# Kernel tuning notes

Measured on AMD Instinct MI355X. Metric: run time of the kernel, lower is better.

Reference implementation:

```python
import jax, jax.numpy as jnp
import numpy as np

N = 16384       # num nodes
E = 65536       # num edges (before self loops)
IN_DIM = 1536
HID = 1024
HEADS = 8
HD = HID // HEADS  # 128
NEG_SLOPE = 0.2
EPS = 1e-5


def _xavier(key, shape):
    fan_in, fan_out = shape[0], shape[-1]
    s = jnp.sqrt(6.0 / (fan_in + fan_out)).astype(jnp.float32)
    return jax.random.uniform(key, shape, jnp.float32, -s, s)


def setup_inputs() -> dict:
    key = jax.random.key(0)
    ks = jax.random.split(key, 32)
    inp = {
        "x": jax.random.normal(ks[0], (N, IN_DIM), jnp.float32),
        "edge_index": jax.random.randint(ks[1], (2, E), 0, N, dtype=jnp.int32),
        # input projection + norm1
        "W_in": _xavier(ks[2], (IN_DIM, HID)), "b_in": jnp.zeros((HID,), jnp.float32),
        "ln1_g": jnp.ones((HID,), jnp.float32), "ln1_b": jnp.zeros((HID,), jnp.float32),
        # GATv2 layer 1
        "g1_Wl": _xavier(ks[3], (HID, HID)), "g1_bl": jnp.zeros((HID,), jnp.float32),
        "g1_Wr": _xavier(ks[4], (HID, HID)), "g1_br": jnp.zeros((HID,), jnp.float32),
        "g1_att": _xavier(ks[5], (HEADS, HD)), "g1_bo": jnp.zeros((HID,), jnp.float32),
        "ln2_g": jnp.ones((HID,), jnp.float32), "ln2_b": jnp.zeros((HID,), jnp.float32),
        # GATv2 layer 2
        "g2_Wl": _xavier(ks[6], (HID, HID)), "g2_bl": jnp.zeros((HID,), jnp.float32),
        "g2_Wr": _xavier(ks[7], (HID, HID)), "g2_br": jnp.zeros((HID,), jnp.float32),
        "g2_att": _xavier(ks[8], (HEADS, HD)), "g2_bo": jnp.zeros((HID,), jnp.float32),
        "ln3_g": jnp.ones((HID,), jnp.float32), "ln3_b": jnp.zeros((HID,), jnp.float32),
        # scorer MLP 1024 -> 512 -> 128 -> 1
        "Ws1": _xavier(ks[9], (HID, 512)), "bs1": jnp.zeros((512,), jnp.float32),
        "Ws2": _xavier(ks[10], (512, 128)), "bs2": jnp.zeros((128,), jnp.float32),
        "Ws3": _xavier(ks[11], (128, 1)), "bs3": jnp.zeros((1,), jnp.float32),
    }
    return inp


def layer_norm(x, g, b):
    mu = jnp.mean(x, axis=-1, keepdims=True)
    var = jnp.var(x, axis=-1, keepdims=True)
    return (x - mu) * jax.lax.rsqrt(var + EPS) * g + b


def gatv2(h, src, dst, Wl, bl, Wr, br, att, bo):
    # GATv2Conv: x_j = lin_l(h)[src], x_i = lin_r(h)[dst]
    xl = (h @ Wl + bl).reshape(N, HEADS, HD)
    xr = (h @ Wr + br).reshape(N, HEADS, HD)
    e = jax.nn.leaky_relu(xl[src] + xr[dst], NEG_SLOPE)      # [E', H, C]
    logit = jnp.einsum('ehc,hc->eh', e, att)                  # [E', H]
    m = jax.ops.segment_max(logit, dst, num_segments=N)       # segment softmax over dst
    a = jnp.exp(logit - m[dst])
    denom = jax.ops.segment_sum(a, dst, num_segments=N)
    alpha = a / denom[dst]
    out = jax.ops.segment_sum(alpha[:, :, None] * xl[src], dst, num_segments=N)
    return out.reshape(N, HID) + bo


def reference(x, edge_index, W_in, b_in, ln1_g, ln1_b,
              g1_Wl, g1_bl, g1_Wr, g1_br, g1_att, g1_bo, ln2_g, ln2_b,
              g2_Wl, g2_bl, g2_Wr, g2_br, g2_att, g2_bo, ln3_g, ln3_b,
              Ws1, bs1, Ws2, bs2, Ws3, bs3):
    # PyG GATv2Conv adds self-loops by default
    loop = jnp.arange(N, dtype=edge_index.dtype)
    src = jnp.concatenate([edge_index[0], loop])
    dst = jnp.concatenate([edge_index[1], loop])

    h = jax.nn.gelu(layer_norm(x @ W_in + b_in, ln1_g, ln1_b), approximate=False)
    h1 = gatv2(h, src, dst, g1_Wl, g1_bl, g1_Wr, g1_br, g1_att, g1_bo)
    h = h + jax.nn.gelu(layer_norm(h1, ln2_g, ln2_b), approximate=False)
    h2 = gatv2(h, src, dst, g2_Wl, g2_bl, g2_Wr, g2_br, g2_att, g2_bo)
    h = h + jax.nn.gelu(layer_norm(h2, ln3_g, ln3_b), approximate=False)

    s = jax.nn.silu(h @ Ws1 + bs1)
    s = jax.nn.silu(s @ Ws2 + bs2)
    scores = (s @ Ws3 + bs3).squeeze(-1)   # [N]
    return scores, h
```

## Files before the change

kernel.cpp:

```cpp
#include <hip/hip_runtime.h>
#include <hip/hip_bf16.h>
#include <math.h>

#define N_NODES 16384
#define E_EDGES 65536
#define ET (E_EDGES + N_NODES)
#define IN_DIM 1536
#define HID 1024
#define XSTR 2048

typedef __attribute__((ext_vector_type(8))) short bf16x8;
typedef __attribute__((ext_vector_type(4))) float f32x4;

__device__ __forceinline__ unsigned short f2b(float f) {
  unsigned int u = __float_as_uint(f);
  u = (u + 0x7FFFu + ((u >> 16) & 1u)) >> 16;
  return (unsigned short)u;
}

__device__ __forceinline__ float b2f(unsigned short u) {
  return __uint_as_float((unsigned int)u << 16);
}

__device__ __forceinline__ void gload_lds16(const void* g, void* l) {
  __builtin_amdgcn_global_load_lds((const __attribute__((address_space(1))) void*)g,
                                   (__attribute__((address_space(3))) void*)l, 16, 0, 0);
}

__device__ __forceinline__ float gelu_exact(float y) {
  return 0.5f * y * (1.0f + erff(y * 0.70710678118654752f));
}

__global__ void conv_bf16_kernel(const float* __restrict__ in, unsigned short* __restrict__ out, int n4) {
  int i = blockIdx.x * 256 + threadIdx.x;
  if (i < n4) {
    float4 v = ((const float4*)in)[i];
    ushort4 o;
    o.x = f2b(v.x); o.y = f2b(v.y); o.z = f2b(v.z); o.w = f2b(v.w);
    ((ushort4*)out)[i] = o;
  }
}

__global__ void transpose_conv_kernel(const float* __restrict__ in, unsigned short* __restrict__ out,
                                      int K, int N) {
  __shared__ float tile[32][33];
  int bx = blockIdx.x * 32;
  int by = blockIdx.y * 32;
  int tx = threadIdx.x, ty = threadIdx.y;
  #pragma unroll
  for (int i = 0; i < 32; i += 8)
    tile[ty + i][tx] = in[(size_t)(by + ty + i) * N + bx + tx];
  __syncthreads();
  #pragma unroll
  for (int i = 0; i < 32; i += 8)
    out[(size_t)(bx + ty + i) * K + by + tx] = f2b(tile[tx][ty + i]);
}

__global__ void concat2_kernel(const float* __restrict__ a, const float* __restrict__ b,
                               float* __restrict__ o, int n) {
  int i = blockIdx.x * 256 + threadIdx.x;
  if (i < n) o[i] = a[i];
  else if (i < 2 * n) o[i] = b[i - n];
}

template <int ACT, int WB>
__global__ __launch_bounds__(512)
void gemm_bf16_kernel(const unsigned short* __restrict__ A, const unsigned short* __restrict__ Bt,
                      const float* __restrict__ bias, float* __restrict__ C,
                      unsigned short* __restrict__ Cb, int M, int N, int K, int nx) {
  __shared__ unsigned short As[256 * 64];
  __shared__ unsigned short Bs[128 * 64];
  const int t = threadIdx.x;
  const int l = t & 63;
  const int w = t >> 6;
  const int wr = w >> 1, wc = w & 1;

  const int nwg = gridDim.x;
  const int bid = blockIdx.x;
  int tile = bid;
  if ((nwg & 7) == 0) {
    const int cpx = nwg >> 3;
    tile = (bid & 7) * cpx + (bid >> 3);
  }
  const int bm = (tile / nx) * 256;
  const int bn = (tile % nx) * 128;

  f32x4 acc[4][4];
  #pragma unroll
  for (int m = 0; m < 4; m++)
    #pragma unroll
    for (int n = 0; n < 4; n++) acc[m][n] = (f32x4){0.f, 0.f, 0.f, 0.f};

  const int srow = t >> 3;
  const int scolbsw = ((t & 7) * 16) ^ ((srow & 7) << 4);
  const unsigned short* Ag = A + (size_t)(bm + srow) * K + (scolbsw >> 1);
  const unsigned short* Bg = Bt + (size_t)(bn + srow) * K + (scolbsw >> 1);

  const int ar = wr * 64 + (l & 15);
  const int br = wc * 64 + (l & 15);
  const int kk2 = (l >> 4) * 16;
  const int swA = (ar & 7) << 4;
  const int swB = (br & 7) << 4;
  const char* Asb = (const char*)As;
  const char* Bsb = (const char*)Bs;

  for (int k0 = 0; k0 < K; k0 += 64) {
    #pragma unroll
    for (int i = 0; i < 4; i++)
      gload_lds16(Ag + (size_t)i * 64 * K + k0, (char*)As + t * 16 + i * 8192);
    #pragma unroll
    for (int i = 0; i < 2; i++)
      gload_lds16(Bg + (size_t)i * 64 * K + k0, (char*)Bs + t * 16 + i * 8192);
    __syncthreads();
    bf16x8 af[4], bfr[4];
    #pragma unroll
    for (int kh = 0; kh < 2; kh++) {
      const int kb = kk2 + kh * 64;
      #pragma unroll
      for (int m = 0; m < 4; m++)
        af[m] = *(const bf16x8*)(Asb + (ar + m * 16) * 128 + (kb ^ swA));
      #pragma unroll
      for (int n = 0; n < 4; n++)
        bfr[n] = *(const bf16x8*)(Bsb + (br + n * 16) * 128 + (kb ^ swB));
      #pragma unroll
      for (int m = 0; m < 4; m++)
        #pragma unroll
        for (int n = 0; n < 4; n++)
          acc[m][n] = __builtin_amdgcn_mfma_f32_16x16x32_bf16(af[m], bfr[n], acc[m][n], 0, 0, 0);
    }
    __syncthreads();
  }

  const int crow0 = bm + wr * 64 + (l >> 4) * 4;
  const int ccol0 = bn + wc * 64 + (l & 15);
  #pragma unroll
  for (int m = 0; m < 4; m++) {
    #pragma unroll
    for (int n = 0; n < 4; n++) {
      int col = ccol0 + n * 16;
      float bv = bias[col];
      #pragma unroll
      for (int v = 0; v < 4; v++) {
        int row = crow0 + m * 16 + v;
        float x = acc[m][n][v] + bv;
        if (ACT == 1) x = x / (1.0f + expf(-x));
        if (WB != 2) C[(size_t)row * N + col] = x;
        if (WB != 0) Cb[(size_t)row * N + col] = f2b(x);
      }
    }
  }
}

__global__ __launch_bounds__(256)
void ln_gelu_kernel(const float* __restrict__ c, const float* __restrict__ g,
                    const float* __restrict__ b, float* __restrict__ h,
                    unsigned short* __restrict__ hb) {
  int row = blockIdx.x;
  int t = threadIdx.x;
  const float* cr = c + (size_t)row * HID;
  float v[4];
  float s = 0.f, q = 0.f;
  #pragma unroll
  for (int j = 0; j < 4; j++) {
    v[j] = cr[t + 256 * j];
    s += v[j];
    q += v[j] * v[j];
  }
  #pragma unroll
  for (int off = 32; off; off >>= 1) {
    s += __shfl_xor(s, off);
    q += __shfl_xor(q, off);
  }
  __shared__ float rs[4], rq[4];
  int wv = t >> 6, l = t & 63;
  if (l == 0) { rs[wv] = s; rq[wv] = q; }
  __syncthreads();
  s = rs[0] + rs[1] + rs[2] + rs[3];
  q = rq[0] + rq[1] + rq[2] + rq[3];
  float mu = s * (1.0f / HID);
  float var = q * (1.0f / HID) - mu * mu;
  float rstd = rsqrtf(var + 1e-5f);
  float* hr = h + (size_t)row * HID;
  unsigned short* hbr = hb + (size_t)row * HID;
  #pragma unroll
  for (int j = 0; j < 4; j++) {
    int ci = t + 256 * j;
    float y = (v[j] - mu) * rstd * g[ci] + b[ci];
    float z = gelu_exact(y);
    hr[ci] = z;
    hbr[ci] = f2b(z);
  }
}

__global__ void build_edges_kernel(const int* __restrict__ ei, int* __restrict__ srcA,
                                   int* __restrict__ dstA, int* __restrict__ deg) {
  int i = blockIdx.x * 256 + threadIdx.x;
  if (i >= ET) return;
  int s, d;
  if (i < E_EDGES) { s = ei[i]; d = ei[E_EDGES + i]; }
  else             { s = i - E_EDGES; d = s; }
  srcA[i] = s;
  dstA[i] = d;
  atomicAdd(&deg[d], 1);
}

__global__ __launch_bounds__(1024)
void scan16k_kernel(const int* __restrict__ deg, int* __restrict__ rowstart) {
  __shared__ int s[1024];
  int t = threadIdx.x;
  int local[16];
  int sum = 0;
  #pragma unroll
  for (int i = 0; i < 16; i++) { local[i] = deg[t * 16 + i]; sum += local[i]; }
  s[t] = sum;
  __syncthreads();
  for (int off = 1; off < 1024; off <<= 1) {
    int v = (t >= off) ? s[t - off] : 0;
    __syncthreads();
    s[t] += v;
    __syncthreads();
  }
  int run = s[t] - sum;
  #pragma unroll
  for (int i = 0; i < 16; i++) { rowstart[t * 16 + i] = run; run += local[i]; }
  if (t == 1023) rowstart[16384] = run;
}

__global__ void scatter_edges_kernel(const int* __restrict__ srcA, const int* __restrict__ dstA,
                                     const int* __restrict__ rowstart, int* __restrict__ cursor,
                                     int* __restrict__ src_csr) {
  int i = blockIdx.x * 256 + threadIdx.x;
  if (i >= ET) return;
  int d = dstA[i];
  int pos = atomicAdd(&cursor[d], 1);
  src_csr[rowstart[d] + pos] = srcA[i];
}

__global__ __launch_bounds__(256)
void gat_fused_kernel(const unsigned short* __restrict__ xe, const float* __restrict__ att,
                      const int* __restrict__ src_csr, const int* __restrict__ rowstart,
                      const float* __restrict__ bo, const float* __restrict__ lng,
                      const float* __restrict__ lnb, float* __restrict__ h,
                      unsigned short* __restrict__ hb) {
  const int l = threadIdx.x & 63;
  const int nid = blockIdx.x * 4 + (threadIdx.x >> 6);
  const int beg = rowstart[nid], end = rowstart[nid + 1];
  const int cb = l * 16;

  float xrf[16], attf[16];
  {
    const unsigned short* xrd = xe + (size_t)nid * XSTR + 1024 + cb;
    bf16x8 r0 = *(const bf16x8*)xrd;
    bf16x8 r1 = *(const bf16x8*)(xrd + 8);
    #pragma unroll
    for (int j = 0; j < 8; j++) {
      xrf[j] = b2f((unsigned short)r0[j]);
      xrf[j + 8] = b2f((unsigned short)r1[j]);
    }
    #pragma unroll
    for (int j = 0; j < 4; j++) {
      float4 a = *(const float4*)(att + cb + j * 4);
      attf[j * 4] = a.x; attf[j * 4 + 1] = a.y;
      attf[j * 4 + 2] = a.z; attf[j * 4 + 3] = a.w;
    }
  }

  float m = -1e30f, den = 0.f;
  float acc[16];
  #pragma unroll
  for (int j = 0; j < 16; j++) acc[j] = 0.f;

  bf16x8 x0, x1;
  if (beg < end) {
    const unsigned short* xls = xe + (size_t)src_csr[beg] * XSTR + cb;
    x0 = *(const bf16x8*)xls;
    x1 = *(const bf16x8*)(xls + 8);
  }
  for (int e = beg; e < end; ++e) {
    bf16x8 c0 = x0, c1 = x1;
    if (e + 1 < end) {
      const unsigned short* xls = xe + (size_t)src_csr[e + 1] * XSTR + cb;
      x0 = *(const bf16x8*)xls;
      x1 = *(const bf16x8*)(xls + 8);
    }
    float xf[16];
    #pragma unroll
    for (int j = 0; j < 8; j++) {
      xf[j] = b2f((unsigned short)c0[j]);
      xf[j + 8] = b2f((unsigned short)c1[j]);
    }
    float p = 0.f;
    #pragma unroll
    for (int j = 0; j < 16; j++) {
      float u = xf[j] + xrf[j];
      u = u > 0.f ? u : 0.2f * u;
      p += u * attf[j];
    }
    p += __shfl_xor(p, 1);
    p += __shfl_xor(p, 2);
    p += __shfl_xor(p, 4);
    float nm = fmaxf(m, p);
    float sc = expf(m - nm);
    float wgt = expf(p - nm);
    den = den * sc + wgt;
    #pragma unroll
    for (int j = 0; j < 16; j++) acc[j] = acc[j] * sc + wgt * xf[j];
    m = nm;
  }

  float inv = 1.0f / den;
  float v[16];
  #pragma unroll
  for (int j = 0; j < 4; j++) {
    float4 b = *(const float4*)(bo + cb + j * 4);
    v[j * 4] = acc[j * 4] * inv + b.x;
    v[j * 4 + 1] = acc[j * 4 + 1] * inv + b.y;
    v[j * 4 + 2] = acc[j * 4 + 2] * inv + b.z;
    v[j * 4 + 3] = acc[j * 4 + 3] * inv + b.w;
  }
  float s = 0.f, q = 0.f;
  #pragma unroll
  for (int j = 0; j < 16; j++) { s += v[j]; q += v[j] * v[j]; }
  #pragma unroll
  for (int off = 32; off; off >>= 1) {
    s += __shfl_xor(s, off);
    q += __shfl_xor(q, off);
  }
  float mu = s * (1.0f / HID);
  float var = q * (1.0f / HID) - mu * mu;
  float rstd = rsqrtf(var + 1e-5f);

  float* hr = h + (size_t)nid * HID + cb;
  unsigned short* hbr = hb + (size_t)nid * HID + cb;
  #pragma unroll
  for (int j = 0; j < 4; j++) {
    float4 gv = *(const float4*)(lng + cb + j * 4);
    float4 bb = *(const float4*)(lnb + cb + j * 4);
    float4 hold = *(const float4*)(hr + j * 4);
    float o0 = hold.x + gelu_exact((v[j * 4] - mu) * rstd * gv.x + bb.x);
    float o1 = hold.y + gelu_exact((v[j * 4 + 1] - mu) * rstd * gv.y + bb.y);
    float o2 = hold.z + gelu_exact((v[j * 4 + 2] - mu) * rstd * gv.z + bb.z);
    float o3 = hold.w + gelu_exact((v[j * 4 + 3] - mu) * rstd * gv.w + bb.w);
    *(float4*)(hr + j * 4) = (float4){o0, o1, o2, o3};
    ushort4 ob;
    ob.x = f2b(o0); ob.y = f2b(o1); ob.z = f2b(o2); ob.w = f2b(o3);
    *(ushort4*)(hbr + j * 4) = ob;
  }
}

__global__ __launch_bounds__(256)
void score_kernel(const float* __restrict__ s2, const float* __restrict__ Ws3,
                  const float* __restrict__ bs3, float* __restrict__ out) {
  int nid = blockIdx.x * 4 + (threadIdx.x >> 6);
  int l = threadIdx.x & 63;
  const float* r = s2 + (size_t)nid * 128;
  float a = r[l] * Ws3[l] + r[l + 64] * Ws3[l + 64];
  #pragma unroll
  for (int off = 32; off; off >>= 1) a += __shfl_xor(a, off);
  if (l == 0) out[nid] = a + bs3[0];
}

extern "C" void kernel_launch(void* const* d_in, const int* in_sizes, int n_in,
                              void* d_out, int out_size, void* d_ws, size_t ws_size,
                              hipStream_t stream) {
  const float* x    = (const float*)d_in[0];
  const int*   ei   = (const int*)  d_in[1];
  const float* W_in = (const float*)d_in[2];
  const float* b_in = (const float*)d_in[3];
  const float* ln1g = (const float*)d_in[4];
  const float* ln1b = (const float*)d_in[5];
  const float* g1Wl = (const float*)d_in[6];
  const float* g1bl = (const float*)d_in[7];
  const float* g1Wr = (const float*)d_in[8];
  const float* g1br = (const float*)d_in[9];
  const float* g1att= (const float*)d_in[10];
  const float* g1bo = (const float*)d_in[11];
  const float* ln2g = (const float*)d_in[12];
  const float* ln2b = (const float*)d_in[13];
  const float* g2Wl = (const float*)d_in[14];
  const float* g2bl = (const float*)d_in[15];
  const float* g2Wr = (const float*)d_in[16];
  const float* g2br = (const float*)d_in[17];
  const float* g2att= (const float*)d_in[18];
  const float* g2bo = (const float*)d_in[19];
  const float* ln3g = (const float*)d_in[20];
  const float* ln3b = (const float*)d_in[21];
  const float* Ws1  = (const float*)d_in[22];
  const float* bs1  = (const float*)d_in[23];
  const float* Ws2  = (const float*)d_in[24];
  const float* bs2  = (const float*)d_in[25];
  const float* Ws3  = (const float*)d_in[26];
  const float* bs3  = (const float*)d_in[27];

  float* scores = (float*)d_out;
  float* h      = (float*)d_out + N_NODES;

  char* wsp = (char*)d_ws;
  size_t off = 0;
  auto alloc = [&](size_t bytes) -> char* {
    char* p = wsp + off;
    off += (bytes + 255) & ~(size_t)255;
    return p;
  };
  unsigned short* xb    = (unsigned short*)alloc((size_t)N_NODES * IN_DIM * 2);
  unsigned short* WinT  = (unsigned short*)alloc((size_t)HID * IN_DIM * 2);
  unsigned short* g1WT  = (unsigned short*)alloc((size_t)XSTR * HID * 2);
  unsigned short* g2WT  = (unsigned short*)alloc((size_t)XSTR * HID * 2);
  unsigned short* Ws1T  = (unsigned short*)alloc((size_t)512 * HID * 2);
  unsigned short* Ws2T  = (unsigned short*)alloc((size_t)128 * 512 * 2);
  unsigned short* hb    = (unsigned short*)alloc((size_t)N_NODES * HID * 2);
  unsigned short* s1b   = (unsigned short*)alloc((size_t)N_NODES * 512 * 2);
  unsigned short* xe    = (unsigned short*)alloc((size_t)N_NODES * XSTR * 2);
  float* bcat1  = (float*)alloc((size_t)XSTR * 4);
  float* bcat2  = (float*)alloc((size_t)XSTR * 4);
  float* C      = (float*)alloc((size_t)N_NODES * HID * 4);
  int* srcA     = (int*)alloc((size_t)ET * 4);
  int* dstA     = (int*)alloc((size_t)ET * 4);
  int* deg      = (int*)alloc(65536);
  int* cursor   = (int*)alloc(65536);
  int* rowstart = (int*)alloc(65544);
  int* src_csr  = (int*)alloc((size_t)ET * 4);

  conv_bf16_kernel<<<(N_NODES * IN_DIM / 4 + 255) / 256, 256, 0, stream>>>(x, xb, N_NODES * IN_DIM / 4);
  dim3 tb(32, 8);
  transpose_conv_kernel<<<dim3(HID / 32, IN_DIM / 32), tb, 0, stream>>>(W_in, WinT, IN_DIM, HID);
  transpose_conv_kernel<<<dim3(HID / 32, HID / 32), tb, 0, stream>>>(g1Wl, g1WT, HID, HID);
  transpose_conv_kernel<<<dim3(HID / 32, HID / 32), tb, 0, stream>>>(g1Wr, g1WT + (size_t)HID * HID, HID, HID);
  transpose_conv_kernel<<<dim3(HID / 32, HID / 32), tb, 0, stream>>>(g2Wl, g2WT, HID, HID);
  transpose_conv_kernel<<<dim3(HID / 32, HID / 32), tb, 0, stream>>>(g2Wr, g2WT + (size_t)HID * HID, HID, HID);
  transpose_conv_kernel<<<dim3(512 / 32, HID / 32), tb, 0, stream>>>(Ws1, Ws1T, HID, 512);
  transpose_conv_kernel<<<dim3(128 / 32, 512 / 32), tb, 0, stream>>>(Ws2, Ws2T, 512, 128);
  concat2_kernel<<<XSTR / 256, 256, 0, stream>>>(g1bl, g1br, bcat1, HID);
  concat2_kernel<<<XSTR / 256, 256, 0, stream>>>(g2bl, g2br, bcat2, HID);

  hipMemsetAsync(deg, 0, 131072, stream);
  build_edges_kernel<<<ET / 256, 256, 0, stream>>>(ei, srcA, dstA, deg);
  scan16k_kernel<<<1, 1024, 0, stream>>>(deg, rowstart);
  scatter_edges_kernel<<<ET / 256, 256, 0, stream>>>(srcA, dstA, rowstart, cursor, src_csr);

  gemm_bf16_kernel<0, 0><<<(N_NODES / 256) * (HID / 128), 512, 0, stream>>>(
      xb, WinT, b_in, C, nullptr, N_NODES, HID, IN_DIM, HID / 128);
  ln_gelu_kernel<<<N_NODES, 256, 0, stream>>>(C, ln1g, ln1b, h, hb);

  gemm_bf16_kernel<0, 2><<<(N_NODES / 256) * (XSTR / 128), 512, 0, stream>>>(
      hb, g1WT, bcat1, nullptr, xe, N_NODES, XSTR, HID, XSTR / 128);
  gat_fused_kernel<<<N_NODES / 4, 256, 0, stream>>>(xe, g1att, src_csr, rowstart, g1bo,
                                                    ln2g, ln2b, h, hb);

  gemm_bf16_kernel<0, 2><<<(N_NODES / 256) * (XSTR / 128), 512, 0, stream>>>(
      hb, g2WT, bcat2, nullptr, xe, N_NODES, XSTR, HID, XSTR / 128);
  gat_fused_kernel<<<N_NODES / 4, 256, 0, stream>>>(xe, g2att, src_csr, rowstart, g2bo,
                                                    ln3g, ln3b, h, hb);

  gemm_bf16_kernel<1, 2><<<(N_NODES / 256) * (512 / 128), 512, 0, stream>>>(
      hb, Ws1T, bs1, nullptr, s1b, N_NODES, 512, HID, 512 / 128);
  gemm_bf16_kernel<1, 0><<<(N_NODES / 256) * 1, 512, 0, stream>>>(
      s1b, Ws2T, bs2, C, nullptr, N_NODES, 128, 512, 1);
  score_kernel<<<N_NODES / 4, 256, 0, stream>>>(C, Ws3, bs3, scores);
}
```

Before: 499.4 us.

## Merge weight transposes into one launch, drop bias concat, deepen GAT prefetch

All seven weight transpose-convert launches are folded into a single kernel that picks its matrix by block index. The two bias-concat kernels are removed; the GEMM instead selects between two bias pointers at a split column. The GAT edge loop now prefetches two edges ahead and uses a lazy online softmax that skips the rescale while the new logit stays within a margin of the running max. These changes aim to cut launch overhead and gather latency, and to remove exp/multiply work per edge. The cost is a per-column branch in the GEMM epilogue and extra registers in the GAT kernel.

```diff
diff --git a/kernel.cpp b/kernel.cpp
--- a/kernel.cpp
+++ b/kernel.cpp
@@ -41,33 +41,42 @@
   }
 }
 
-__global__ void transpose_conv_kernel(const float* __restrict__ in, unsigned short* __restrict__ out,
-                                      int K, int N) {
-  __shared__ float tile[32][33];
-  int bx = blockIdx.x * 32;
-  int by = blockIdx.y * 32;
+__global__ void transpose_all_kernel(const float* __restrict__ W_in,
+                                     const float* __restrict__ g1Wl, const float* __restrict__ g1Wr,
+                                     const float* __restrict__ g2Wl, const float* __restrict__ g2Wr,
+                                     const float* __restrict__ Ws1, const float* __restrict__ Ws2,
+                                     unsigned short* __restrict__ WinT, unsigned short* __restrict__ g1WT,
+                                     unsigned short* __restrict__ g2WT, unsigned short* __restrict__ Ws1T,
+                                     unsigned short* __restrict__ Ws2T) {
+  int bid = blockIdx.x;
+  const float* src; unsigned short* dst; int K, N, tile;
+  if (bid < 1536)      { src = W_in; dst = WinT;                          K = 1536; N = 1024; tile = bid; }
+  else if (bid < 2560) { src = g1Wl; dst = g1WT;                         K = 1024; N = 1024; tile = bid - 1536; }
+  else if (bid < 3584) { src = g1Wr; dst = g1WT + (size_t)1024 * 1024;   K = 1024; N = 1024; tile = bid - 2560; }
+  else if (bid < 4608) { src = g2Wl; dst = g2WT;                         K = 1024; N = 1024; tile = bid - 3584; }
+  else if (bid < 5632) { src = g2Wr; dst = g2WT + (size_t)1024 * 1024;   K = 1024; N = 1024; tile = bid - 4608; }
+  else if (bid < 6144) { src = Ws1; dst = Ws1T;                          K = 1024; N = 512;  tile = bid - 5632; }
+  else                 { src = Ws2; dst = Ws2T;                          K = 512;  N = 128;  tile = bid - 6144; }
+  int nxt = N >> 5;
+  int bx = (tile % nxt) * 32;
+  int by = (tile / nxt) * 32;
+  __shared__ float tilebuf[32][33];
   int tx = threadIdx.x, ty = threadIdx.y;
   #pragma unroll
   for (int i = 0; i < 32; i += 8)
-    tile[ty + i][tx] = in[(size_t)(by + ty + i) * N + bx + tx];
+    tilebuf[ty + i][tx] = src[(size_t)(by + ty + i) * N + bx + tx];
   __syncthreads();
   #pragma unroll
   for (int i = 0; i < 32; i += 8)
-    out[(size_t)(bx + ty + i) * K + by + tx] = f2b(tile[tx][ty + i]);
-}
-
-__global__ void concat2_kernel(const float* __restrict__ a, const float* __restrict__ b,
-                               float* __restrict__ o, int n) {
-  int i = blockIdx.x * 256 + threadIdx.x;
-  if (i < n) o[i] = a[i];
-  else if (i < 2 * n) o[i] = b[i - n];
+    dst[(size_t)(bx + ty + i) * K + by + tx] = f2b(tilebuf[tx][ty + i]);
 }
 
 template <int ACT, int WB>
 __global__ __launch_bounds__(512)
 void gemm_bf16_kernel(const unsigned short* __restrict__ A, const unsigned short* __restrict__ Bt,
-                      const float* __restrict__ bias, float* __restrict__ C,
-                      unsigned short* __restrict__ Cb, int M, int N, int K, int nx) {
+                      const float* __restrict__ bias, const float* __restrict__ bias2, int nsplit,
+                      float* __restrict__ C, unsigned short* __restrict__ Cb,
+                      int M, int N, int K, int nx) {
   __shared__ unsigned short As[256 * 64];
   __shared__ unsigned short Bs[128 * 64];
   const int t = threadIdx.x;
@@ -138,7 +147,7 @@
     #pragma unroll
     for (int n = 0; n < 4; n++) {
       int col = ccol0 + n * 16;
-      float bv = bias[col];
+      float bv = (col < nsplit) ? bias[col] : bias2[col - nsplit];
       #pragma unroll
       for (int v = 0; v < 4; v++) {
         int row = crow0 + m * 16 + v;
@@ -270,18 +279,24 @@
   #pragma unroll
   for (int j = 0; j < 16; j++) acc[j] = 0.f;
 
-  bf16x8 x0, x1;
+  bf16x8 xa0, xa1, xb0, xb1;
   if (beg < end) {
-    const unsigned short* xls = xe + (size_t)src_csr[beg] * XSTR + cb;
-    x0 = *(const bf16x8*)xls;
-    x1 = *(const bf16x8*)(xls + 8);
+    const unsigned short* p = xe + (size_t)src_csr[beg] * XSTR + cb;
+    xa0 = *(const bf16x8*)p;
+    xa1 = *(const bf16x8*)(p + 8);
+  }
+  if (beg + 1 < end) {
+    const unsigned short* p = xe + (size_t)src_csr[beg + 1] * XSTR + cb;
+    xb0 = *(const bf16x8*)p;
+    xb1 = *(const bf16x8*)(p + 8);
   }
   for (int e = beg; e < end; ++e) {
-    bf16x8 c0 = x0, c1 = x1;
-    if (e + 1 < end) {
-      const unsigned short* xls = xe + (size_t)src_csr[e + 1] * XSTR + cb;
-      x0 = *(const bf16x8*)xls;
-      x1 = *(const bf16x8*)(xls + 8);
+    bf16x8 c0 = xa0, c1 = xa1;
+    xa0 = xb0; xa1 = xb1;
+    if (e + 2 < end) {
+      const unsigned short* p = xe + (size_t)src_csr[e + 2] * XSTR + cb;
+      xb0 = *(const bf16x8*)p;
+      xb1 = *(const bf16x8*)(p + 8);
     }
     float xf[16];
     #pragma unroll
@@ -289,23 +304,30 @@
       xf[j] = b2f((unsigned short)c0[j]);
       xf[j + 8] = b2f((unsigned short)c1[j]);
     }
-    float p = 0.f;
+    float lg = 0.f;
     #pragma unroll
     for (int j = 0; j < 16; j++) {
       float u = xf[j] + xrf[j];
-      u = u > 0.f ? u : 0.2f * u;
-      p += u * attf[j];
-    }
-    p += __shfl_xor(p, 1);
-    p += __shfl_xor(p, 2);
-    p += __shfl_xor(p, 4);
-    float nm = fmaxf(m, p);
-    float sc = expf(m - nm);
-    float wgt = expf(p - nm);
-    den = den * sc + wgt;
-    #pragma unroll
-    for (int j = 0; j < 16; j++) acc[j] = acc[j] * sc + wgt * xf[j];
-    m = nm;
+      u = fmaxf(u, 0.2f * u);
+      lg = fmaf(u, attf[j], lg);
+    }
+    lg += __shfl_xor(lg, 1);
+    lg += __shfl_xor(lg, 2);
+    lg += __shfl_xor(lg, 4);
+    if (__all(lg <= m + 8.f)) {
+      float wgt = expf(lg - m);
+      den += wgt;
+      #pragma unroll
+      for (int j = 0; j < 16; j++) acc[j] = fmaf(wgt, xf[j], acc[j]);
+    } else {
+      float nm = fmaxf(m, lg);
+      float sc = expf(m - nm);
+      float wgt = expf(lg - nm);
+      den = den * sc + wgt;
+      #pragma unroll
+      for (int j = 0; j < 16; j++) acc[j] = fmaf(wgt, xf[j], acc[j] * sc);
+      m = nm;
+    }
   }
 
   float inv = 1.0f / den;
@@ -411,8 +433,6 @@
   unsigned short* hb    = (unsigned short*)alloc((size_t)N_NODES * HID * 2);
   unsigned short* s1b   = (unsigned short*)alloc((size_t)N_NODES * 512 * 2);
   unsigned short* xe    = (unsigned short*)alloc((size_t)N_NODES * XSTR * 2);
-  float* bcat1  = (float*)alloc((size_t)XSTR * 4);
-  float* bcat2  = (float*)alloc((size_t)XSTR * 4);
   float* C      = (float*)alloc((size_t)N_NODES * HID * 4);
   int* srcA     = (int*)alloc((size_t)ET * 4);
   int* dstA     = (int*)alloc((size_t)ET * 4);
@@ -422,16 +442,8 @@
   int* src_csr  = (int*)alloc((size_t)ET * 4);
 
   conv_bf16_kernel<<<(N_NODES * IN_DIM / 4 + 255) / 256, 256, 0, stream>>>(x, xb, N_NODES * IN_DIM / 4);
-  dim3 tb(32, 8);
-  transpose_conv_kernel<<<dim3(HID / 32, IN_DIM / 32), tb, 0, stream>>>(W_in, WinT, IN_DIM, HID);
-  transpose_conv_kernel<<<dim3(HID / 32, HID / 32), tb, 0, stream>>>(g1Wl, g1WT, HID, HID);
-  transpose_conv_kernel<<<dim3(HID / 32, HID / 32), tb, 0, stream>>>(g1Wr, g1WT + (size_t)HID * HID, HID, HID);
-  transpose_conv_kernel<<<dim3(HID / 32, HID / 32), tb, 0, stream>>>(g2Wl, g2WT, HID, HID);
-  transpose_conv_kernel<<<dim3(HID / 32, HID / 32), tb, 0, stream>>>(g2Wr, g2WT + (size_t)HID * HID, HID, HID);
-  transpose_conv_kernel<<<dim3(512 / 32, HID / 32), tb, 0, stream>>>(Ws1, Ws1T, HID, 512);
-  transpose_conv_kernel<<<dim3(128 / 32, 512 / 32), tb, 0, stream>>>(Ws2, Ws2T, 512, 128);
-  concat2_kernel<<<XSTR / 256, 256, 0, stream>>>(g1bl, g1br, bcat1, HID);
-  concat2_kernel<<<XSTR / 256, 256, 0, stream>>>(g2bl, g2br, bcat2, HID);
+  transpose_all_kernel<<<6208, dim3(32, 8), 0, stream>>>(W_in, g1Wl, g1Wr, g2Wl, g2Wr, Ws1, Ws2,
+                                                         WinT, g1WT, g2WT, Ws1T, Ws2T);
 
   hipMemsetAsync(deg, 0, 131072, stream);
   build_edges_kernel<<<ET / 256, 256, 0, stream>>>(ei, srcA, dstA, deg);
@@ -439,22 +451,22 @@
   scatter_edges_kernel<<<ET / 256, 256, 0, stream>>>(srcA, dstA, rowstart, cursor, src_csr);
 
   gemm_bf16_kernel<0, 0><<<(N_NODES / 256) * (HID / 128), 512, 0, stream>>>(
-      xb, WinT, b_in, C, nullptr, N_NODES, HID, IN_DIM, HID / 128);
+      xb, WinT, b_in, b_in, HID, C, nullptr, N_NODES, HID, IN_DIM, HID / 128);
   ln_gelu_kernel<<<N_NODES, 256, 0, stream>>>(C, ln1g, ln1b, h, hb);
 
   gemm_bf16_kernel<0, 2><<<(N_NODES / 256) * (XSTR / 128), 512, 0, stream>>>(
-      hb, g1WT, bcat1, nullptr, xe, N_NODES, XSTR, HID, XSTR / 128);
+      hb, g1WT, g1bl, g1br, HID, nullptr, xe, N_NODES, XSTR, HID, XSTR / 128);
   gat_fused_kernel<<<N_NODES / 4, 256, 0, stream>>>(xe, g1att, src_csr, rowstart, g1bo,
                                                     ln2g, ln2b, h, hb);
 
   gemm_bf16_kernel<0, 2><<<(N_NODES / 256) * (XSTR / 128), 512, 0, stream>>>(
-      hb, g2WT, bcat2, nullptr, xe, N_NODES, XSTR, HID, XSTR / 128);
+      hb, g2WT, g2bl, g2br, HID, nullptr, xe, N_NODES, XSTR, HID, XSTR / 128);
   gat_fused_kernel<<<N_NODES / 4, 256, 0, stream>>>(xe, g2att, src_csr, rowstart, g2bo,
                                                     ln3g, ln3b, h, hb);
 
   gemm_bf16_kernel<1, 2><<<(N_NODES / 256) * (512 / 128), 512, 0, stream>>>(
-      hb, Ws1T, bs1, nullptr, s1b, N_NODES, 512, HID, 512 / 128);
+      hb, Ws1T, bs1, bs1, 512, nullptr, s1b, N_NODES, 512, HID, 512 / 128);
   gemm_bf16_kernel<1, 0><<<(N_NODES / 256) * 1, 512, 0, stream>>>(
-      s1b, Ws2T, bs2, C, nullptr, N_NODES, 128, 512, 1);
+      s1b, Ws2T, bs2, bs2, 128, C, nullptr, N_NODES, 128, 512, 1);
   score_kernel<<<N_NODES / 4, 256, 0, stream>>>(C, Ws3, bs3, scores);
 }
```

Measured after the change: 493.0 us. About the same (-1.3%).
